# Kernel tuning notes

Hardware: AMD Instinct MI355X
Metric: run time of the kernel (lower is better)

## Reference

```python
import jax, jax.numpy as jnp
import numpy as np

B, S, D, H = 2, 2048, 1024, 16
DK = D // H


def setup_inputs() -> dict:
    key = jax.random.key(0)
    ks = jax.random.split(key, 7)
    q = jax.random.normal(ks[0], (B, S, D), dtype=jnp.float32)
    k = jax.random.normal(ks[1], (B, S, D), dtype=jnp.float32)
    v = jax.random.normal(ks[2], (B, S, D), dtype=jnp.float32)
    # causal mask, broadcastable [B,1,S,S]; masked_fill where mask==0
    mask = jnp.broadcast_to(jnp.tril(jnp.ones((S, S), dtype=jnp.int32)), (B, 1, S, S))
    scale = 0.02
    Wq = jax.random.normal(ks[3], (D, D), dtype=jnp.float32) * scale
    Wk = jax.random.normal(ks[4], (D, D), dtype=jnp.float32) * scale
    Wv = jax.random.normal(ks[5], (D, D), dtype=jnp.float32) * scale
    Wo = jax.random.normal(ks[6], (D, D), dtype=jnp.float32) * scale
    return {"q": q, "k": k, "v": v, "mask": mask, "Wq": Wq, "Wk": Wk, "Wv": Wv, "Wo": Wo}


def reference(q, k, v, mask, Wq, Wk, Wv, Wo):
    # torch nn.Linear(bias=False): y = x @ W.T with W of shape [out, in]
    def proj(x, W):
        return (x @ W.T).reshape(B, S, H, DK).transpose(0, 2, 1, 3)  # [B,H,S,DK]

    Q = proj(q, Wq)
    K = proj(k, Wk)
    V = proj(v, Wv)
    inv_sqrt_dk = np.float32(1.0 / np.sqrt(DK))
    scores = jnp.einsum('bhqd,bhkd->bhqk', Q, K) * inv_sqrt_dk  # [B,H,S,S]
    scores = jnp.where(mask == 0, jnp.float32(-jnp.inf), scores)
    attn = jax.nn.softmax(scores, axis=-1)
    x = jnp.einsum('bhqk,bhkd->bhqd', attn, V)  # [B,H,S,DK]
    x = x.transpose(0, 2, 1, 3).reshape(B, S, D)
    return x @ Wo.T
```

## Files before the change

kernel.cpp:

```cpp
#include <hip/hip_runtime.h>

typedef __bf16 bf16x8 __attribute__((ext_vector_type(8)));
typedef float  f32x4  __attribute__((ext_vector_type(4)));

#define DEV static __device__ __forceinline__
#define VMCNT(n) asm volatile("s_waitcnt vmcnt(" #n ")" ::: "memory")
#define LGKM0()  asm volatile("s_waitcnt lgkmcnt(0)" ::: "memory")
#define SBAR()   __builtin_amdgcn_s_barrier()
#define SFENCE() __builtin_amdgcn_sched_barrier(0)


DEV ushort f2bf(float f) {
    uint u = __builtin_bit_cast(uint, f);
    u = u + 0x7fffu + ((u >> 16) & 1u);
    return (ushort)(u >> 16);
}

DEV void stage_swz(const ushort* g, int gstride, char* lds, int nchunks) {
    const int tid  = threadIdx.x;
    const int lane = tid & 63;
    const int wave = tid >> 6;
    for (int c0 = wave * 64; c0 < nchunks; c0 += 256) {
        int c   = c0 + lane;
        int row = c >> 3;
        int cc  = (c & 7) ^ (row & 7);
        const ushort* src = g + row * gstride + cc * 8;
        __builtin_amdgcn_global_load_lds((__attribute__((address_space(1))) void*)src,
                                         (__attribute__((address_space(3))) void*)(lds + c0 * 16),
                                         16, 0, 0);
    }
}

DEV bf16x8 ldfrag(const char* tile, int row, int kc) {
    int off = (row << 7) + ((kc ^ (row & 7)) << 4);
    return *(const bf16x8*)(tile + off);
}


struct CvtArgs { const float* s[7]; ushort* d[7]; int n[7]; };

__global__ void cvt_kernel(CvtArgs a) {
    const int y = blockIdx.y;
    const float* __restrict__ s = a.s[y];
    ushort* __restrict__ d = a.d[y];
    const int n = a.n[y];
    const int stride = gridDim.x * blockDim.x;
    for (int i = blockIdx.x * blockDim.x + threadIdx.x; i * 8 < n; i += stride) {
        const float4* p = (const float4*)(s + (size_t)i * 8);
        float4 x = p[0], yv = p[1];
        uint4 o;
        o.x = (uint)f2bf(x.x)  | ((uint)f2bf(x.y)  << 16);
        o.y = (uint)f2bf(x.z)  | ((uint)f2bf(x.w)  << 16);
        o.z = (uint)f2bf(yv.x) | ((uint)f2bf(yv.y) << 16);
        o.w = (uint)f2bf(yv.z) | ((uint)f2bf(yv.w) << 16);
        *(uint4*)(d + (size_t)i * 8) = o;
    }
}


constexpr int GN = 1024, GK = 1024;

template<typename EPI>
DEV void gemm_body(const ushort* __restrict__ A, const ushort* __restrict__ W,
                   char* smem, EPI epi) {
    char* As[2] = { smem,         smem + 16384 };
    char* Ws[2] = { smem + 32768, smem + 40960 };
    const int tid  = threadIdx.x;
    const int lane = tid & 63;
    const int w    = tid >> 6;
    const int wr   = w >> 1, wc = w & 1;
    const int hi   = lane >> 4, lj = lane & 15;
    const int bid  = blockIdx.x;
    const int nb   = bid & 15, mb = bid >> 4;

    f32x4 acc[4][2];
#pragma unroll
    for (int mi = 0; mi < 4; mi++)
#pragma unroll
        for (int ni = 0; ni < 2; ni++) acc[mi][ni] = f32x4{0.f, 0.f, 0.f, 0.f};

    const ushort* Ag = A + (size_t)mb * 128 * GK;
    const ushort* Wg = W + (size_t)nb * 64 * GK;

    stage_swz(Ag, GK, As[0], 1024);
    stage_swz(Wg, GK, Ws[0], 512);
    int cur = 0;
    for (int k0 = 0; k0 < GK; k0 += 64) {
        if (k0 + 64 < GK) {
            stage_swz(Ag + k0 + 64, GK, As[cur ^ 1], 1024);
            stage_swz(Wg + k0 + 64, GK, Ws[cur ^ 1], 512);
            VMCNT(6);
        } else {
            VMCNT(0);
        }
        SBAR(); SFENCE();
#pragma unroll
        for (int kk = 0; kk < 2; ++kk) {
            bf16x8 a[4], b[2];
#pragma unroll
            for (int mi = 0; mi < 4; mi++) a[mi] = ldfrag(As[cur], wr * 64 + mi * 16 + lj, kk * 4 + hi);
#pragma unroll
            for (int ni = 0; ni < 2; ni++) b[ni] = ldfrag(Ws[cur], wc * 32 + ni * 16 + lj, kk * 4 + hi);
#pragma unroll
            for (int mi = 0; mi < 4; mi++)
#pragma unroll
                for (int ni = 0; ni < 2; ni++)
                    acc[mi][ni] = __builtin_amdgcn_mfma_f32_16x16x32_bf16(a[mi], b[ni], acc[mi][ni], 0, 0, 0);
        }
        LGKM0();
        SBAR(); SFENCE();
        cur ^= 1;
    }

#pragma unroll
    for (int mi = 0; mi < 4; mi++)
#pragma unroll
        for (int r = 0; r < 4; r++) {
            const int gm = mb * 128 + wr * 64 + mi * 16 + hi * 4 + r;
#pragma unroll
            for (int ni = 0; ni < 2; ni++) {
                const int gn = nb * 64 + wc * 32 + ni * 16 + lj;
                epi(gm, gn, acc[mi][ni][r]);
            }
        }
}

struct ProjArgs {
    const ushort* A[3]; const ushort* W[3]; ushort* O[3];
    float scale[3]; int mode[3];
};

__global__ __launch_bounds__(256) void gemm_proj(ProjArgs args) {
    __shared__ char smem[49152];
    const int z = blockIdx.z;
    const ushort* A = args.A[z];
    const ushort* W = args.W[z];
    ushort* Out = args.O[z];
    const float scale = args.scale[z];
    const int mode = args.mode[z];
    gemm_body(A, W, smem, [&](int gm, int gn, float v) {
        v *= scale;
        const int b_ = gm >> 11, s_ = gm & 2047;
        const int h_ = gn >> 6,  d_ = gn & 63;
        size_t off;
        if (mode == 0) off = (((size_t)b_ * 16 + h_) * 2048 + s_) * 64 + d_;
        else           off = (((size_t)b_ * 16 + h_) * 64 + d_) * 2048 + s_;
        Out[off] = f2bf(v);
    });
}

__global__ __launch_bounds__(256) void gemm_out(const ushort* __restrict__ A,
                                                const ushort* __restrict__ W,
                                                float* __restrict__ Out) {
    __shared__ char smem[49152];
    gemm_body(A, W, smem, [&](int gm, int gn, float v) {
        Out[(size_t)gm * GN + gn] = v;
    });
}


__global__ __launch_bounds__(256) void attn_kernel(const ushort* __restrict__ Qb,
                                                   const ushort* __restrict__ Kb,
                                                   const ushort* __restrict__ Vt,
                                                   ushort* __restrict__ Xb) {
    constexpr int S = 2048;
    __shared__ char smem[49152];
    const int tid = threadIdx.x, lane = tid & 63, w = tid >> 6;
    const int hi = lane >> 4, lj = lane & 15;
    char* Pw = smem + 32768 + w * 4096;
    const int bh = blockIdx.x;
    const int yraw = blockIdx.y;
    const int qt = (yraw < 8) ? yraw : 23 - yraw;
    const int q0 = qt * 128;
    const int q0w = q0 + w * 32;

    const ushort* Qg = Qb + (size_t)bh * S * 64;
    const ushort* Kg = Kb + (size_t)bh * S * 64;
    const ushort* Vg = Vt + (size_t)bh * 64 * S;

    bf16x8 qf[2][2];
#pragma unroll
    for (int mi = 0; mi < 2; mi++)
#pragma unroll
        for (int kk = 0; kk < 2; kk++)
            qf[mi][kk] = *(const bf16x8*)(Qg + (size_t)(q0w + mi * 16 + lj) * 64 + kk * 32 + hi * 8);

    f32x4 o[2][4];
    float m_run[2] = { -1e30f, -1e30f }, l_run[2] = { 0.f, 0.f };
#pragma unroll
    for (int mi = 0; mi < 2; mi++)
#pragma unroll
        for (int nd = 0; nd < 4; nd++) o[mi][nd] = f32x4{0.f, 0.f, 0.f, 0.f};

    const int nt = qt * 2 + 2;
    stage_swz(Kg, 64, smem, 512);
    stage_swz(Vg, S, smem + 16384, 512);
    int cur = 0;

    for (int t = 0; t < nt; ++t) {
        char* Kc = smem + (cur << 13);
        char* Vc = smem + 16384 + (cur << 13);
        if (t + 1 < nt) {
            stage_swz(Kg + (size_t)(t + 1) * 64 * 64, 64, smem + ((cur ^ 1) << 13), 512);
            stage_swz(Vg + (t + 1) * 64, S, smem + 16384 + ((cur ^ 1) << 13), 512);
            VMCNT(4);
        } else {
            VMCNT(0);
        }
        SBAR(); SFENCE();

        if (t * 64 <= q0w + 31) {
            f32x4 sc[2][4];
#pragma unroll
            for (int mi = 0; mi < 2; mi++)
#pragma unroll
                for (int ni = 0; ni < 4; ni++) sc[mi][ni] = f32x4{0.f, 0.f, 0.f, 0.f};
            __builtin_amdgcn_s_setprio(1);
#pragma unroll
            for (int kk = 0; kk < 2; ++kk) {
                bf16x8 kf[4];
#pragma unroll
                for (int ni = 0; ni < 4; ni++) kf[ni] = ldfrag(Kc, ni * 16 + lj, kk * 4 + hi);
#pragma unroll
                for (int mi = 0; mi < 2; mi++)
#pragma unroll
                    for (int ni = 0; ni < 4; ni++)
                        sc[mi][ni] = __builtin_amdgcn_mfma_f32_16x16x32_bf16(kf[ni], qf[mi][kk], sc[mi][ni], 0, 0, 0);
            }
            __builtin_amdgcn_s_setprio(0);

            const bool diag = (t * 64 + 63 > q0w);
#pragma unroll
            for (int mi = 0; mi < 2; mi++) {
                const int q = q0w + mi * 16 + lj;
                if (diag) {
#pragma unroll
                    for (int ni = 0; ni < 4; ni++)
#pragma unroll
                        for (int r = 0; r < 4; r++)
                            if (t * 64 + ni * 16 + hi * 4 + r > q) sc[mi][ni][r] = -1e30f;
                }
                float mx = -1e30f;
#pragma unroll
                for (int ni = 0; ni < 4; ni++)
#pragma unroll
                    for (int r = 0; r < 4; r++) mx = fmaxf(mx, sc[mi][ni][r]);
                mx = fmaxf(mx, __shfl_xor(mx, 16));
                mx = fmaxf(mx, __shfl_xor(mx, 32));
                const float mo = m_run[mi];
                const float mn = fmaxf(mo, mx);
                const float rs = __expf(mo - mn);
                m_run[mi] = mn;
                float ps = 0.f;
                const int row = mi * 16 + lj;
#pragma unroll
                for (int ni = 0; ni < 4; ni++) {
                    float p0 = __expf(sc[mi][ni][0] - mn);
                    float p1 = __expf(sc[mi][ni][1] - mn);
                    float p2 = __expf(sc[mi][ni][2] - mn);
                    float p3 = __expf(sc[mi][ni][3] - mn);
                    ps += (p0 + p1) + (p2 + p3);
                    uint lo  = (uint)f2bf(p0) | ((uint)f2bf(p1) << 16);
                    uint hi2 = (uint)f2bf(p2) | ((uint)f2bf(p3) << 16);
                    const int c = ni * 2 + (hi >> 1);
                    uint2 pv; pv.x = lo; pv.y = hi2;
                    *(uint2*)(Pw + row * 128 + ((c ^ (row & 7)) << 4) + ((hi & 1) << 3)) = pv;
                }
                ps += __shfl_xor(ps, 16);
                ps += __shfl_xor(ps, 32);
                l_run[mi] = l_run[mi] * rs + ps;
#pragma unroll
                for (int r = 0; r < 4; r++) {
                    float rr = __shfl(rs, (lane & 48) | (hi * 4 + r));
#pragma unroll
                    for (int nd = 0; nd < 4; nd++) o[mi][nd][r] *= rr;
                }
            }

            LGKM0(); SFENCE();

            __builtin_amdgcn_s_setprio(1);
#pragma unroll
            for (int kk = 0; kk < 2; ++kk) {
                bf16x8 pa[2], bv[4];
#pragma unroll
                for (int mi = 0; mi < 2; mi++) pa[mi] = ldfrag(Pw, mi * 16 + lj, kk * 4 + hi);
#pragma unroll
                for (int nd = 0; nd < 4; nd++) bv[nd] = ldfrag(Vc, nd * 16 + lj, kk * 4 + hi);
#pragma unroll
                for (int mi = 0; mi < 2; mi++)
#pragma unroll
                    for (int nd = 0; nd < 4; nd++)
                        o[mi][nd] = __builtin_amdgcn_mfma_f32_16x16x32_bf16(pa[mi], bv[nd], o[mi][nd], 0, 0, 0);
            }
            __builtin_amdgcn_s_setprio(0);
        }

        LGKM0();
        SBAR(); SFENCE();
        cur ^= 1;
    }

    const int b_ = bh >> 4, h_ = bh & 15;
#pragma unroll
    for (int mi = 0; mi < 2; mi++)
#pragma unroll
        for (int r = 0; r < 4; r++) {
            float lv = __shfl(l_run[mi], (lane & 48) | (hi * 4 + r));
            float inv = 1.f / lv;
            const int srow = q0w + mi * 16 + hi * 4 + r;
#pragma unroll
            for (int nd = 0; nd < 4; nd++)
                Xb[((size_t)b_ * S + srow) * 1024 + h_ * 64 + nd * 16 + lj] =
                    f2bf(o[mi][nd][r] * inv);
        }
}


extern "C" void kernel_launch(void* const* d_in, const int* in_sizes, int n_in,
                              void* d_out, int out_size, void* d_ws, size_t ws_size,
                              hipStream_t stream) {
    (void)in_sizes; (void)n_in; (void)out_size; (void)ws_size;
    const float* q  = (const float*)d_in[0];
    const float* k  = (const float*)d_in[1];
    const float* v  = (const float*)d_in[2];
    const float* Wq = (const float*)d_in[4];
    const float* Wk = (const float*)d_in[5];
    const float* Wv = (const float*)d_in[6];
    const float* Wo = (const float*)d_in[7];

    char* ws = (char*)d_ws;
    const size_t MB = (size_t)1 << 20;
    ushort* Qb  = (ushort*)(ws + 0 * MB);
    ushort* Kb  = (ushort*)(ws + 8 * MB);
    ushort* Vtb = (ushort*)(ws + 16 * MB);
    ushort* Xb  = (ushort*)(ws + 24 * MB);
    ushort* qb  = (ushort*)(ws + 32 * MB);
    ushort* kb  = (ushort*)(ws + 40 * MB);
    ushort* vb  = (ushort*)(ws + 48 * MB);
    ushort* Wqb = (ushort*)(ws + 56 * MB);
    ushort* Wkb = (ushort*)(ws + 58 * MB);
    ushort* Wvb = (ushort*)(ws + 60 * MB);
    ushort* Wob = (ushort*)(ws + 62 * MB);

    CvtArgs c;
    c.s[0] = q;  c.s[1] = k;  c.s[2] = v;  c.s[3] = Wq;  c.s[4] = Wk;  c.s[5] = Wv;  c.s[6] = Wo;
    c.d[0] = qb; c.d[1] = kb; c.d[2] = vb; c.d[3] = Wqb; c.d[4] = Wkb; c.d[5] = Wvb; c.d[6] = Wob;
    c.n[0] = c.n[1] = c.n[2] = 4 * 1024 * 1024;
    c.n[3] = c.n[4] = c.n[5] = c.n[6] = 1024 * 1024;
    cvt_kernel<<<dim3(1024, 7), 256, 0, stream>>>(c);

    ProjArgs p;
    p.A[0] = qb;  p.A[1] = kb;  p.A[2] = vb;
    p.W[0] = Wqb; p.W[1] = Wkb; p.W[2] = Wvb;
    p.O[0] = Qb;  p.O[1] = Kb;  p.O[2] = Vtb;
    p.scale[0] = 0.125f; p.scale[1] = 1.0f; p.scale[2] = 1.0f;
    p.mode[0] = 0; p.mode[1] = 0; p.mode[2] = 1;
    gemm_proj<<<dim3(512, 1, 3), 256, 0, stream>>>(p);

    attn_kernel<<<dim3(32, 16), 256, 0, stream>>>(Qb, Kb, Vtb, Xb);

    gemm_out<<<512, 256, 0, stream>>>(Xb, Wob, (float*)d_out);
}
```

Baseline: 282.8 us.

## Enlarge GEMM tiles, use exp2 softmax with lazy rescale, hardware bf16 packing

Several independent changes land together. The projection and output GEMMs move from 128x64 to 128x128 tiles, giving more MFMA reuse per LDS load at the cost of more LDS, more accumulators and half as many blocks. The attention softmax folds log2(e) into the Q scale and uses exp2, and it skips the rescale of O and l whenever the running max grows by at most 8 (a lazy-rescale threshold). The attention q-tile order is reversed so the heaviest causal tiles launch first, and bf16 conversion uses native packed casts instead of manual rounding.

New measurement: 262.0 us. 1.08x faster.

```diff
diff --git a/kernel.cpp b/kernel.cpp
--- a/kernel.cpp
+++ b/kernel.cpp
@@ -1,6 +1,7 @@
 #include <hip/hip_runtime.h>
 
 typedef __bf16 bf16x8 __attribute__((ext_vector_type(8)));
+typedef __bf16 bf16x2 __attribute__((ext_vector_type(2)));
 typedef float  f32x4  __attribute__((ext_vector_type(4)));
 
 #define DEV static __device__ __forceinline__
@@ -11,9 +12,11 @@
 
 
 DEV ushort f2bf(float f) {
-    uint u = __builtin_bit_cast(uint, f);
-    u = u + 0x7fffu + ((u >> 16) & 1u);
-    return (ushort)(u >> 16);
+    return __builtin_bit_cast(ushort, (__bf16)f);
+}
+DEV uint pk2(float a, float b) {
+    bf16x2 t; t[0] = (__bf16)a; t[1] = (__bf16)b;
+    return __builtin_bit_cast(uint, t);
 }
 
 DEV void stage_swz(const ushort* g, int gstride, char* lds, int nchunks) {
@@ -49,10 +52,10 @@
         const float4* p = (const float4*)(s + (size_t)i * 8);
         float4 x = p[0], yv = p[1];
         uint4 o;
-        o.x = (uint)f2bf(x.x)  | ((uint)f2bf(x.y)  << 16);
-        o.y = (uint)f2bf(x.z)  | ((uint)f2bf(x.w)  << 16);
-        o.z = (uint)f2bf(yv.x) | ((uint)f2bf(yv.y) << 16);
-        o.w = (uint)f2bf(yv.z) | ((uint)f2bf(yv.w) << 16);
+        o.x = pk2(x.x,  x.y);
+        o.y = pk2(x.z,  x.w);
+        o.z = pk2(yv.x, yv.y);
+        o.w = pk2(yv.z, yv.w);
         *(uint4*)(d + (size_t)i * 8) = o;
     }
 }
@@ -63,48 +66,47 @@
 template<typename EPI>
 DEV void gemm_body(const ushort* __restrict__ A, const ushort* __restrict__ W,
                    char* smem, EPI epi) {
-    char* As[2] = { smem,         smem + 16384 };
-    char* Ws[2] = { smem + 32768, smem + 40960 };
     const int tid  = threadIdx.x;
     const int lane = tid & 63;
     const int w    = tid >> 6;
     const int wr   = w >> 1, wc = w & 1;
     const int hi   = lane >> 4, lj = lane & 15;
-    const int bid  = blockIdx.x;
-    const int nb   = bid & 15, mb = bid >> 4;
-
-    f32x4 acc[4][2];
+    const int nb   = blockIdx.x & 7, mb = blockIdx.x >> 3;
+
+    f32x4 acc[4][4];
 #pragma unroll
     for (int mi = 0; mi < 4; mi++)
 #pragma unroll
-        for (int ni = 0; ni < 2; ni++) acc[mi][ni] = f32x4{0.f, 0.f, 0.f, 0.f};
+        for (int ni = 0; ni < 4; ni++) acc[mi][ni] = f32x4{0.f, 0.f, 0.f, 0.f};
 
     const ushort* Ag = A + (size_t)mb * 128 * GK;
-    const ushort* Wg = W + (size_t)nb * 64 * GK;
-
-    stage_swz(Ag, GK, As[0], 1024);
-    stage_swz(Wg, GK, Ws[0], 512);
+    const ushort* Wg = W + (size_t)nb * 128 * GK;
+
+    stage_swz(Ag, GK, smem, 1024);
+    stage_swz(Wg, GK, smem + 32768, 1024);
     int cur = 0;
     for (int k0 = 0; k0 < GK; k0 += 64) {
+        char* Ac = smem + (cur << 14);
+        char* Wc = smem + 32768 + (cur << 14);
         if (k0 + 64 < GK) {
-            stage_swz(Ag + k0 + 64, GK, As[cur ^ 1], 1024);
-            stage_swz(Wg + k0 + 64, GK, Ws[cur ^ 1], 512);
-            VMCNT(6);
+            stage_swz(Ag + k0 + 64, GK, smem + ((cur ^ 1) << 14), 1024);
+            stage_swz(Wg + k0 + 64, GK, smem + 32768 + ((cur ^ 1) << 14), 1024);
+            VMCNT(8);
         } else {
             VMCNT(0);
         }
         SBAR(); SFENCE();
 #pragma unroll
         for (int kk = 0; kk < 2; ++kk) {
-            bf16x8 a[4], b[2];
-#pragma unroll
-            for (int mi = 0; mi < 4; mi++) a[mi] = ldfrag(As[cur], wr * 64 + mi * 16 + lj, kk * 4 + hi);
-#pragma unroll
-            for (int ni = 0; ni < 2; ni++) b[ni] = ldfrag(Ws[cur], wc * 32 + ni * 16 + lj, kk * 4 + hi);
+            bf16x8 a[4], b[4];
+#pragma unroll
+            for (int mi = 0; mi < 4; mi++) a[mi] = ldfrag(Ac, wr * 64 + mi * 16 + lj, kk * 4 + hi);
+#pragma unroll
+            for (int ni = 0; ni < 4; ni++) b[ni] = ldfrag(Wc, wc * 64 + ni * 16 + lj, kk * 4 + hi);
 #pragma unroll
             for (int mi = 0; mi < 4; mi++)
 #pragma unroll
-                for (int ni = 0; ni < 2; ni++)
+                for (int ni = 0; ni < 4; ni++)
                     acc[mi][ni] = __builtin_amdgcn_mfma_f32_16x16x32_bf16(a[mi], b[ni], acc[mi][ni], 0, 0, 0);
         }
         LGKM0();
@@ -118,8 +120,8 @@
         for (int r = 0; r < 4; r++) {
             const int gm = mb * 128 + wr * 64 + mi * 16 + hi * 4 + r;
 #pragma unroll
-            for (int ni = 0; ni < 2; ni++) {
-                const int gn = nb * 64 + wc * 32 + ni * 16 + lj;
+            for (int ni = 0; ni < 4; ni++) {
+                const int gn = nb * 128 + wc * 64 + ni * 16 + lj;
                 epi(gm, gn, acc[mi][ni][r]);
             }
         }
@@ -131,7 +133,7 @@
 };
 
 __global__ __launch_bounds__(256) void gemm_proj(ProjArgs args) {
-    __shared__ char smem[49152];
+    __shared__ char smem[65536];
     const int z = blockIdx.z;
     const ushort* A = args.A[z];
     const ushort* W = args.W[z];
@@ -152,7 +154,7 @@
 __global__ __launch_bounds__(256) void gemm_out(const ushort* __restrict__ A,
                                                 const ushort* __restrict__ W,
                                                 float* __restrict__ Out) {
-    __shared__ char smem[49152];
+    __shared__ char smem[65536];
     gemm_body(A, W, smem, [&](int gm, int gn, float v) {
         Out[(size_t)gm * GN + gn] = v;
     });
@@ -170,7 +172,7 @@
     char* Pw = smem + 32768 + w * 4096;
     const int bh = blockIdx.x;
     const int yraw = blockIdx.y;
-    const int qt = (yraw < 8) ? yraw : 23 - yraw;
+    const int qt = (yraw < 8) ? 15 - yraw : yraw - 8;
     const int q0 = qt * 128;
     const int q0w = q0 + w * 32;
 
@@ -248,32 +250,35 @@
                 mx = fmaxf(mx, __shfl_xor(mx, 16));
                 mx = fmaxf(mx, __shfl_xor(mx, 32));
                 const float mo = m_run[mi];
-                const float mn = fmaxf(mo, mx);
-                const float rs = __expf(mo - mn);
-                m_run[mi] = mn;
+                const bool defer = __all(mx <= mo + 8.f);
+                float mn, rs;
+                if (defer) { mn = mo; rs = 1.f; }
+                else { mn = fmaxf(mo, mx); rs = __builtin_exp2f(mo - mn); m_run[mi] = mn; }
                 float ps = 0.f;
                 const int row = mi * 16 + lj;
 #pragma unroll
                 for (int ni = 0; ni < 4; ni++) {
-                    float p0 = __expf(sc[mi][ni][0] - mn);
-                    float p1 = __expf(sc[mi][ni][1] - mn);
-                    float p2 = __expf(sc[mi][ni][2] - mn);
-                    float p3 = __expf(sc[mi][ni][3] - mn);
+                    float p0 = __builtin_exp2f(sc[mi][ni][0] - mn);
+                    float p1 = __builtin_exp2f(sc[mi][ni][1] - mn);
+                    float p2 = __builtin_exp2f(sc[mi][ni][2] - mn);
+                    float p3 = __builtin_exp2f(sc[mi][ni][3] - mn);
                     ps += (p0 + p1) + (p2 + p3);
-                    uint lo  = (uint)f2bf(p0) | ((uint)f2bf(p1) << 16);
-                    uint hi2 = (uint)f2bf(p2) | ((uint)f2bf(p3) << 16);
+                    uint2 pv; pv.x = pk2(p0, p1); pv.y = pk2(p2, p3);
                     const int c = ni * 2 + (hi >> 1);
-                    uint2 pv; pv.x = lo; pv.y = hi2;
                     *(uint2*)(Pw + row * 128 + ((c ^ (row & 7)) << 4) + ((hi & 1) << 3)) = pv;
                 }
                 ps += __shfl_xor(ps, 16);
                 ps += __shfl_xor(ps, 32);
-                l_run[mi] = l_run[mi] * rs + ps;
-#pragma unroll
-                for (int r = 0; r < 4; r++) {
-                    float rr = __shfl(rs, (lane & 48) | (hi * 4 + r));
-#pragma unroll
-                    for (int nd = 0; nd < 4; nd++) o[mi][nd][r] *= rr;
+                if (defer) {
+                    l_run[mi] += ps;
+                } else {
+                    l_run[mi] = l_run[mi] * rs + ps;
+#pragma unroll
+                    for (int r = 0; r < 4; r++) {
+                        float rr = __shfl(rs, (lane & 48) | (hi * 4 + r));
+#pragma unroll
+                        for (int nd = 0; nd < 4; nd++) o[mi][nd][r] *= rr;
+                    }
                 }
             }
 
@@ -354,11 +359,12 @@
     p.A[0] = qb;  p.A[1] = kb;  p.A[2] = vb;
     p.W[0] = Wqb; p.W[1] = Wkb; p.W[2] = Wvb;
     p.O[0] = Qb;  p.O[1] = Kb;  p.O[2] = Vtb;
-    p.scale[0] = 0.125f; p.scale[1] = 1.0f; p.scale[2] = 1.0f;
+    p.scale[0] = 0.125f * 1.44269504088896f;
+    p.scale[1] = 1.0f; p.scale[2] = 1.0f;
     p.mode[0] = 0; p.mode[1] = 0; p.mode[2] = 1;
-    gemm_proj<<<dim3(512, 1, 3), 256, 0, stream>>>(p);
+    gemm_proj<<<dim3(256, 1, 3), 256, 0, stream>>>(p);
 
     attn_kernel<<<dim3(32, 16), 256, 0, stream>>>(Qb, Kb, Vtb, Xb);
 
-    gemm_out<<<512, 256, 0, stream>>>(Xb, Wob, (float*)d_out);
-}
+    gemm_out<<<256, 256, 0, stream>>>(Xb, Wob, (float*)d_out);
+}
```
